# Optimization experiments

Measured on AMD Instinct MI355X. Metric: run time of the kernel, lower is better.

## Reference

```python
import jax, jax.numpy as jnp
import numpy as np
import math

B, S, D = 4, 4096, 512

def setup_inputs() -> dict:
    key = jax.random.key(0)
    k_tok, k1, k2, k3 = jax.random.split(key, 4)
    scale = 1.0 / math.sqrt(D)
    return {
        "token": jax.random.normal(k_tok, (B, S, D), dtype=jnp.float32),
        "W1": jax.random.normal(k1, (D, D), dtype=jnp.float32) * scale,
        "W2": jax.random.normal(k2, (D, D), dtype=jnp.float32) * scale,
        "W3": jax.random.normal(k3, (D, D), dtype=jnp.float32) * scale,
    }

def reference(token, W1, W2, W3):
    # nn.Linear(dim, dim, bias=False): y = x @ W.T; W stored as [out, in]
    q = jnp.einsum('bsd,ed->bse', token, W1)  # t1(token)
    k = jnp.einsum('bsd,ed->bse', token, W2)  # t2(token)
    v = jnp.einsum('bsd,ed->bse', token, W3)  # t3(token)
    logits = jnp.einsum('bse,bte->bst', q, k) / jnp.sqrt(jnp.float32(token.shape[-1]))
    scores = jax.nn.softmax(logits, axis=-1)  # full [B,S,S] materialized, as in source
    return jnp.einsum('bst,bte->bse', scores, v)
```

## Files before the change

kernel.cpp:

```cpp
#include <hip/hip_runtime.h>
#include <stdint.h>


#define BDIM 4
#define SDIM 4096
#define DDIM 512
#define MROWS (BDIM * SDIM)
#define XB_ELEMS ((size_t)MROWS * DDIM)
#define W_ELEMS ((size_t)DDIM * DDIM)

typedef short short8_t __attribute__((ext_vector_type(8)));
typedef short short4_t __attribute__((ext_vector_type(4)));
typedef float float4_t __attribute__((ext_vector_type(4)));

typedef __attribute__((address_space(1))) void gvoid_t;
typedef __attribute__((address_space(3))) void lvoid_t;

__device__ __forceinline__ short f2bf(float f) {
    union { float f; uint32_t u; } v; v.f = f;
    uint32_t r = v.u + 0x7FFFu + ((v.u >> 16) & 1u);
    return (short)(r >> 16);
}
__device__ __forceinline__ float bf2f(short s) {
    union { uint32_t u; float f; } v; v.u = ((uint32_t)(uint16_t)s) << 16;
    return v.f;
}

__global__ void detect_kernel(const uint32_t* __restrict__ tok, int* __restrict__ flag) {
    __shared__ int red[256];
    const int tid = threadIdx.x;
    int c = 0;
    for (int i = tid; i < 4096; i += 256) {
        uint32_t e = (tok[i] >> 7) & 0xFFu;
        c += (e >= 105u && e <= 135u) ? 1 : 0;
    }
    red[tid] = c;
    __syncthreads();
    for (int s = 128; s > 0; s >>= 1) {
        if (tid < s) red[tid] += red[tid + s];
        __syncthreads();
    }
    if (tid == 0) *flag = (red[0] > 2048) ? 1 : 0;
}

__global__ void zero_rs_kernel(float* __restrict__ RS) {
    RS[blockIdx.x * 256 + threadIdx.x] = 0.f;
}

__global__ void convert_kernel(const void* __restrict__ X, const void* __restrict__ W1,
                               const void* __restrict__ W2, const void* __restrict__ W3,
                               short* __restrict__ dst, const int* __restrict__ flagp)
{
    const int bf16in = *flagp;
    const size_t i4 = ((size_t)blockIdx.x * 256 + threadIdx.x) * 4;
    const void* src; size_t off;
    if (i4 < XB_ELEMS) { src = X; off = i4; }
    else {
        const size_t j = i4 - XB_ELEMS;
        const int g = (int)(j / W_ELEMS);
        src = (g == 0) ? W1 : (g == 1) ? W2 : W3;
        off = j - (size_t)g * W_ELEMS;
    }
    if (bf16in) {
        *(short4_t*)(dst + i4) = *(const short4_t*)((const short*)src + off);
    } else {
        float4 v = *(const float4*)((const float*)src + off);
        short4_t s = { f2bf(v.x), f2bf(v.y), f2bf(v.z), f2bf(v.w) };
        *(short4_t*)(dst + i4) = s;
    }
}

__device__ __forceinline__ void gemm_core(
    const short* __restrict__ A, int lda,
    const short* __restrict__ B, int ldb,
    int m0, int n0, int kIters,
    short* As, short* Bs, float4_t acc[4][4])
{
    const int tid = threadIdx.x;
    const int w = tid >> 6, lane = tid & 63, quad = lane >> 4, l16 = lane & 15;
    const int wm = w >> 1, wn = w & 1;
    const int rsub = lane >> 2;
    const int col8 = 8 * (lane & 3);

    for (int kk = 0; kk < kIters; ++kk) {
        const int k0 = 32 * kk;
        __syncthreads();
#pragma unroll
        for (int c = 0; c < 2; ++c) {
            const int row = 32 * w + 16 * c + rsub;
            const short* g = A + (size_t)(m0 + row) * lda + k0 + col8;
            __builtin_amdgcn_global_load_lds((const gvoid_t*)g,
                (lvoid_t*)(As + (32 * w + 16 * c) * 32), 16, 0, 0);
        }
#pragma unroll
        for (int c = 0; c < 2; ++c) {
            const int row = 32 * w + 16 * c + rsub;
            const short* g = B + (size_t)(n0 + row) * ldb + k0 + col8;
            __builtin_amdgcn_global_load_lds((const gvoid_t*)g,
                (lvoid_t*)(Bs + (32 * w + 16 * c) * 32), 16, 0, 0);
        }
        __syncthreads();

        short8_t af[4], bfr[4];
#pragma unroll
        for (int mt = 0; mt < 4; ++mt)
            af[mt] = *(const short8_t*)&As[(64 * wm + 16 * mt + l16) * 32 + 8 * quad];
#pragma unroll
        for (int nt = 0; nt < 4; ++nt)
            bfr[nt] = *(const short8_t*)&Bs[(64 * wn + 16 * nt + l16) * 32 + 8 * quad];
#pragma unroll
        for (int mt = 0; mt < 4; ++mt)
#pragma unroll
            for (int nt = 0; nt < 4; ++nt)
                acc[mt][nt] = __builtin_amdgcn_mfma_f32_16x16x32_bf16(af[mt], bfr[nt], acc[mt][nt], 0, 0, 0);
    }
}

__global__ void proj_fast(const short* __restrict__ XbWb, short* __restrict__ QKV)
{
    __shared__ __align__(16) short As[128 * 32];
    __shared__ __align__(16) short Bs[128 * 32];

    const short* Xb = XbWb;
    const int bid = blockIdx.x;
    const int g = bid >> 9;
    const int r = bid & 511;

    const short* Ap; const short* Bp; short* Op;
    int m0, n0, ldo;
    if (g == 2) {
        Ap = XbWb + XB_ELEMS + 2 * W_ELEMS; Bp = Xb;
        Op = QKV + 2 * (size_t)MROWS * DDIM;
        m0 = 128 * (r & 3); n0 = 128 * (r >> 2); ldo = MROWS;
    } else {
        Ap = Xb; Bp = XbWb + XB_ELEMS + (size_t)g * W_ELEMS;
        Op = QKV + (size_t)g * MROWS * DDIM;
        m0 = 128 * (r >> 2); n0 = 128 * (r & 3); ldo = DDIM;
    }

    const float4_t z4 = {0.f, 0.f, 0.f, 0.f};
    float4_t acc[4][4];
#pragma unroll
    for (int i = 0; i < 4; ++i)
#pragma unroll
        for (int j = 0; j < 4; ++j) acc[i][j] = z4;

    gemm_core(Ap, DDIM, Bp, DDIM, m0, n0, 16, As, Bs, acc);

    const int tid = threadIdx.x;
    const int w = tid >> 6, lane = tid & 63, quad = lane >> 4, l16 = lane & 15;
    const int wm = w >> 1, wn = w & 1;
#pragma unroll
    for (int mt = 0; mt < 4; ++mt)
#pragma unroll
        for (int nt = 0; nt < 4; ++nt)
#pragma unroll
            for (int rr = 0; rr < 4; ++rr) {
                const int m = m0 + 64 * wm + 16 * mt + 4 * quad + rr;
                const int n = n0 + 64 * wn + 16 * nt + l16;
                Op[(size_t)m * ldo + n] = f2bf(acc[mt][nt][rr]);
            }
}

__global__ void qkt_kernel(const short* __restrict__ QKV, short* __restrict__ P,
                           float* __restrict__ RS, int bbase)
{
    __shared__ __align__(16) short As[128 * 32];
    __shared__ __align__(16) short Bs[128 * 32];

    const int bid = blockIdx.x;
    const int bb = bid >> 10;
    const int r = bid & 1023;
    const int b = bbase + bb;
    const int m0 = 128 * (r >> 5);
    const int n0 = 128 * (r & 31);

    const short* Qb = QKV + (size_t)b * SDIM * DDIM;
    const short* Kb = QKV + (size_t)MROWS * DDIM + (size_t)b * SDIM * DDIM;

    const float4_t z4 = {0.f, 0.f, 0.f, 0.f};
    float4_t acc[4][4];
#pragma unroll
    for (int i = 0; i < 4; ++i)
#pragma unroll
        for (int j = 0; j < 4; ++j) acc[i][j] = z4;

    gemm_core(Qb, DDIM, Kb, DDIM, m0, n0, 16, As, Bs, acc);

    const int tid = threadIdx.x;
    const int w = tid >> 6, lane = tid & 63, quad = lane >> 4, l16 = lane & 15;
    const int wm = w >> 1, wn = w & 1;
    const float kSc = 1.44269504088896341f * 0.04419417382415922f;
    short* Pb = P + (size_t)bb * SDIM * SDIM;
#pragma unroll
    for (int mt = 0; mt < 4; ++mt)
#pragma unroll
        for (int rr = 0; rr < 4; ++rr) {
            const int q = m0 + 64 * wm + 16 * mt + 4 * quad + rr;
            float sum = 0.f;
#pragma unroll
            for (int nt = 0; nt < 4; ++nt) {
                const float p = exp2f(acc[mt][nt][rr] * kSc);
                const short pb = f2bf(p);
                sum += bf2f(pb);
                Pb[(size_t)q * SDIM + n0 + 64 * wn + 16 * nt + l16] = pb;
            }
            sum += __shfl_xor(sum, 1); sum += __shfl_xor(sum, 2);
            sum += __shfl_xor(sum, 4); sum += __shfl_xor(sum, 8);
            if (l16 == 0) atomicAdd(&RS[(size_t)b * SDIM + q], sum);
        }
}

__global__ void pv_kernel(const short* __restrict__ P, const short* __restrict__ QKV,
                          const float* __restrict__ RS, void* __restrict__ out,
                          const int* __restrict__ flagp, int bbase)
{
    __shared__ __align__(16) short As[128 * 32];
    __shared__ __align__(16) short Bs[128 * 32];

    const int bf16out = *flagp;
    const int bid = blockIdx.x;
    const int bb = bid >> 7;
    const int r = bid & 127;
    const int b = bbase + bb;
    const int m0 = 128 * (r >> 2);
    const int n0 = 128 * (r & 3);

    const short* Pb = P + (size_t)bb * SDIM * SDIM;
    const short* Vt = QKV + 2 * (size_t)MROWS * DDIM + (size_t)b * SDIM;

    const float4_t z4 = {0.f, 0.f, 0.f, 0.f};
    float4_t acc[4][4];
#pragma unroll
    for (int i = 0; i < 4; ++i)
#pragma unroll
        for (int j = 0; j < 4; ++j) acc[i][j] = z4;

    gemm_core(Pb, SDIM, Vt, MROWS, m0, n0, 128, As, Bs, acc);

    const int tid = threadIdx.x;
    const int w = tid >> 6, lane = tid & 63, quad = lane >> 4, l16 = lane & 15;
    const int wm = w >> 1, wn = w & 1;
#pragma unroll
    for (int mt = 0; mt < 4; ++mt)
#pragma unroll
        for (int rr = 0; rr < 4; ++rr) {
            const size_t grow = (size_t)b * SDIM + m0 + 64 * wm + 16 * mt + 4 * quad + rr;
            const float inv = 1.0f / RS[grow];
#pragma unroll
            for (int nt = 0; nt < 4; ++nt) {
                const int n = n0 + 64 * wn + 16 * nt + l16;
                const float o = acc[mt][nt][rr] * inv;
                if (bf16out) ((short*)out)[grow * DDIM + n] = f2bf(o);
                else         ((float*)out)[grow * DDIM + n] = o;
            }
        }
}

__global__ void proj_mfma_legacy(const void* __restrict__ X, const void* __restrict__ W1,
                          const void* __restrict__ W2, const void* __restrict__ W3,
                          short* __restrict__ QKV, const int* __restrict__ flagp)
{
    __shared__ __align__(16) short As[128][40];
    __shared__ __align__(16) short Bs[128][40];

    const int bf16in = *flagp;
    const int bid = blockIdx.x;
    const int g = bid >> 9;
    const int r = bid & 511;

    const void* Ap; const void* Bp; short* Op;
    int m0, n0, ldo;
    if (g == 2) {
        Ap = W3; Bp = X; Op = QKV + 2 * (size_t)MROWS * DDIM;
        m0 = 128 * (r & 3); n0 = 128 * (r >> 2); ldo = MROWS;
    } else {
        Ap = X; Bp = (g == 0) ? W1 : W2; Op = QKV + (size_t)g * MROWS * DDIM;
        m0 = 128 * (r >> 2); n0 = 128 * (r & 3); ldo = DDIM;
    }

    const float* Af = (const float*)Ap;  const float* Bf = (const float*)Bp;
    const short* Ah = (const short*)Ap;  const short* Bh = (const short*)Bp;

    const int tid = threadIdx.x;
    const int w = tid >> 6, lane = tid & 63, quad = lane >> 4, l16 = lane & 15;
    const int wm = w >> 1, wn = w & 1;
    const int rgrp = tid >> 3, cg = tid & 7;

    const float4_t z4 = {0.f, 0.f, 0.f, 0.f};
    float4_t acc[4][4];
#pragma unroll
    for (int i = 0; i < 4; ++i)
#pragma unroll
        for (int j = 0; j < 4; ++j) acc[i][j] = z4;

    for (int kk = 0; kk < 16; ++kk) {
        const int k0 = 32 * kk;
        __syncthreads();
        if (bf16in) {
#pragma unroll
            for (int i = 0; i < 4; ++i) {
                const int row = rgrp + 32 * i;
                *(short4_t*)&As[row][4 * cg] =
                    *(const short4_t*)(Ah + (size_t)(m0 + row) * DDIM + k0 + 4 * cg);
                *(short4_t*)&Bs[row][4 * cg] =
                    *(const short4_t*)(Bh + (size_t)(n0 + row) * DDIM + k0 + 4 * cg);
            }
        } else {
#pragma unroll
            for (int i = 0; i < 4; ++i) {
                const int row = rgrp + 32 * i;
                float4 va = *(const float4*)(Af + (size_t)(m0 + row) * DDIM + k0 + 4 * cg);
                short4_t sa = { f2bf(va.x), f2bf(va.y), f2bf(va.z), f2bf(va.w) };
                *(short4_t*)&As[row][4 * cg] = sa;
                float4 vb = *(const float4*)(Bf + (size_t)(n0 + row) * DDIM + k0 + 4 * cg);
                short4_t sb = { f2bf(vb.x), f2bf(vb.y), f2bf(vb.z), f2bf(vb.w) };
                *(short4_t*)&Bs[row][4 * cg] = sb;
            }
        }
        __syncthreads();

        short8_t af[4], bfr[4];
#pragma unroll
        for (int mt = 0; mt < 4; ++mt)
            af[mt] = *(const short8_t*)&As[64 * wm + 16 * mt + l16][8 * quad];
#pragma unroll
        for (int nt = 0; nt < 4; ++nt)
            bfr[nt] = *(const short8_t*)&Bs[64 * wn + 16 * nt + l16][8 * quad];
#pragma unroll
        for (int mt = 0; mt < 4; ++mt)
#pragma unroll
            for (int nt = 0; nt < 4; ++nt)
                acc[mt][nt] = __builtin_amdgcn_mfma_f32_16x16x32_bf16(af[mt], bfr[nt], acc[mt][nt], 0, 0, 0);
    }

#pragma unroll
    for (int mt = 0; mt < 4; ++mt)
#pragma unroll
        for (int nt = 0; nt < 4; ++nt)
#pragma unroll
            for (int rr = 0; rr < 4; ++rr) {
                const int m = m0 + 64 * wm + 16 * mt + 4 * quad + rr;
                const int n = n0 + 64 * wn + 16 * nt + l16;
                Op[(size_t)m * ldo + n] = f2bf(acc[mt][nt][rr]);
            }
}

__global__ void attn_mfma(const short* __restrict__ QKV, void* __restrict__ out,
                          const int* __restrict__ flagp)
{
    __shared__ __align__(16) short Ks[32][520];
    __shared__ __align__(16) short Ps[32][72];
    __shared__ float rowsum[2][32];

    const int bf16out = *flagp;
    const short* Qb = QKV;
    const short* Kb = QKV + (size_t)MROWS * DDIM;
    const short* Vt = QKV + 2 * (size_t)MROWS * DDIM;

    const int b = blockIdx.x >> 7;
    const int q0 = (blockIdx.x & 127) * 32;
    const int tid = threadIdx.x;
    const int w = tid >> 6, lane = tid & 63, quad = lane >> 4, l16 = lane & 15;
    const int strip = w >> 1, half = w & 1;

    short8_t qf[16];
    {
        const short* qrow = Qb + (size_t)(b * SDIM + q0 + 16 * strip + l16) * DDIM + 8 * quad;
#pragma unroll
        for (int kc = 0; kc < 16; ++kc)
            qf[kc] = *(const short8_t*)(qrow + 32 * kc);
    }

    const float4_t z4 = {0.f, 0.f, 0.f, 0.f};
    float4_t o[2][8];
#pragma unroll
    for (int mt = 0; mt < 2; ++mt)
#pragma unroll
        for (int nt = 0; nt < 8; ++nt) o[mt][nt] = z4;
    float rs[4] = {0.f, 0.f, 0.f, 0.f};

    const float kSc = 1.44269504088896341f * 0.04419417382415922f;

    for (int kt = 0; kt < 128; ++kt) {
        const int kv0 = 32 * kt;
        __syncthreads();
#pragma unroll
        for (int r = 0; r < 8; ++r) {
            const int kv = 8 * w + r;
            short8_t t = *(const short8_t*)(Kb + (size_t)(b * SDIM + kv0 + kv) * DDIM + 8 * lane);
            *(short8_t*)&Ks[kv][8 * lane] = t;
        }
        __syncthreads();

        float4_t sacc = z4;
#pragma unroll
        for (int kc = 0; kc < 16; ++kc) {
            short8_t kf = *(const short8_t*)&Ks[16 * half + l16][32 * kc + 8 * quad];
            sacc = __builtin_amdgcn_mfma_f32_16x16x32_bf16(qf[kc], kf, sacc, 0, 0, 0);
        }

#pragma unroll
        for (int r = 0; r < 4; ++r) {
            const float p = exp2f(sacc[r] * kSc);
            const short pb = f2bf(p);
            rs[r] += bf2f(pb);
            Ps[16 * strip + 4 * quad + r][16 * half + l16] = pb;
        }
        __syncthreads();

        short8_t pa0 = *(const short8_t*)&Ps[l16][8 * quad];
        short8_t pa1 = *(const short8_t*)&Ps[16 + l16][8 * quad];
#pragma unroll
        for (int nt = 0; nt < 8; ++nt) {
            const short* vp = Vt + (size_t)(128 * w + 16 * nt + l16) * MROWS
                            + (b * SDIM + kv0 + 8 * quad);
            short8_t vb = *(const short8_t*)vp;
            o[0][nt] = __builtin_amdgcn_mfma_f32_16x16x32_bf16(pa0, vb, o[0][nt], 0, 0, 0);
            o[1][nt] = __builtin_amdgcn_mfma_f32_16x16x32_bf16(pa1, vb, o[1][nt], 0, 0, 0);
        }
    }

#pragma unroll
    for (int r = 0; r < 4; ++r) {
        float v = rs[r];
        v += __shfl_xor(v, 1); v += __shfl_xor(v, 2);
        v += __shfl_xor(v, 4); v += __shfl_xor(v, 8);
        rs[r] = v;
    }
    if (l16 == 0) {
#pragma unroll
        for (int r = 0; r < 4; ++r)
            rowsum[half][16 * strip + 4 * quad + r] = rs[r];
    }
    __syncthreads();

#pragma unroll
    for (int mt = 0; mt < 2; ++mt)
#pragma unroll
        for (int r = 0; r < 4; ++r) {
            const int q = 16 * mt + 4 * quad + r;
            const float inv = 1.0f / (rowsum[0][q] + rowsum[1][q]);
            const size_t base = (size_t)(b * SDIM + q0 + q) * DDIM + 128 * w + l16;
            if (bf16out) {
                short* orow = (short*)out + base;
#pragma unroll
                for (int nt = 0; nt < 8; ++nt)
                    orow[16 * nt] = f2bf(o[mt][nt][r] * inv);
            } else {
                float* orow = (float*)out + base;
#pragma unroll
                for (int nt = 0; nt < 8; ++nt)
                    orow[16 * nt] = o[mt][nt][r] * inv;
            }
        }
}

__global__ void zero_out_kernel(short* __restrict__ out, int n) {
    int i = blockIdx.x * 256 + threadIdx.x;
    if (i < n) out[i] = 0;
}

extern "C" void kernel_launch(void* const* d_in, const int* in_sizes, int n_in,
                              void* d_out, int out_size, void* d_ws, size_t ws_size,
                              hipStream_t stream) {
    const void* token = d_in[0];
    const void* Wp[3] = { d_in[1], d_in[2], d_in[3] };
    {
        int wi = 0;
        const void* tk = nullptr; const void* ws3[3] = {nullptr, nullptr, nullptr};
        bool ok = true;
        for (int i = 0; i < n_in && i < 4; ++i) {
            if (in_sizes[i] == BDIM * SDIM * DDIM) { if (tk) ok = false; tk = d_in[i]; }
            else if (in_sizes[i] == DDIM * DDIM) { if (wi < 3) ws3[wi++] = d_in[i]; else ok = false; }
            else ok = false;
        }
        if (ok && tk && wi == 3) { token = tk; Wp[0] = ws3[0]; Wp[1] = ws3[1]; Wp[2] = ws3[2]; }
    }

    const size_t qkvBytes = 3 * (size_t)MROWS * DDIM * sizeof(short);
    const size_t need_base = qkvBytes + 256;
    if (ws_size < need_base) {
        zero_out_kernel<<<(out_size + 255) / 256, 256, 0, stream>>>((short*)d_out, out_size);
        return;
    }

    short* QKV = (short*)d_ws;
    int* flag = (int*)((char*)d_ws + qkvBytes);
    short* P = (short*)((char*)d_ws + need_base);
    const size_t pElems1 = (size_t)SDIM * SDIM;

    int nb = 0;
    for (int cand = 4; cand >= 1; cand >>= 1) {
        const size_t need = need_base + (size_t)cand * pElems1 * sizeof(short)
                          + (size_t)MROWS * sizeof(float);
        if (ws_size >= need) { nb = cand; break; }
    }

    detect_kernel<<<1, 256, 0, stream>>>((const uint32_t*)token, flag);

    if (nb == 0) {
        proj_mfma_legacy<<<dim3(1536), 256, 0, stream>>>(token, Wp[0], Wp[1], Wp[2], QKV, flag);
        attn_mfma<<<dim3(512), 256, 0, stream>>>(QKV, d_out, flag);
        return;
    }

    short* XbWb = P;
    const size_t cvt4 = (XB_ELEMS + 3 * W_ELEMS) / 4;
    convert_kernel<<<dim3((unsigned)(cvt4 / 256)), 256, 0, stream>>>(
        token, Wp[0], Wp[1], Wp[2], XbWb, flag);
    proj_fast<<<dim3(1536), 256, 0, stream>>>(XbWb, QKV);

    float* RS = (float*)(P + (size_t)nb * pElems1);
    zero_rs_kernel<<<dim3(MROWS / 256), 256, 0, stream>>>(RS);
    for (int p = 0; p < BDIM / nb; ++p) {
        const int bbase = p * nb;
        qkt_kernel<<<dim3(nb * 1024), 256, 0, stream>>>(QKV, P, RS, bbase);
        pv_kernel<<<dim3(nb * 128), 256, 0, stream>>>(P, QKV, RS, d_out, flag, bbase);
    }
}
```

Before: 354.6 us.

## Replace QK^T kernel with 256x256 tiled, 8-wave pipelined LDS-direct MFMA kernel

Replaces the 128x128 QK^T tile kernel with a 256x256 tile kernel that uses 512 threads and 128KB of dynamic LDS. The K dimension is split into 64-wide stages, double-buffered through global_load_lds with swizzled layouts and interleaved barriers. The block index is remapped so consecutive blocks spread across XCDs. The larger tile raises reuse of each loaded tile per FLOP and overlaps loads with MFMA, at the cost of fewer, heavier blocks and more register pressure for the 8x4 accumulators.

```diff
diff --git a/kernel.cpp b/kernel.cpp
--- a/kernel.cpp
+++ b/kernel.cpp
@@ -8,6 +8,7 @@
 #define MROWS (BDIM * SDIM)
 #define XB_ELEMS ((size_t)MROWS * DDIM)
 #define W_ELEMS ((size_t)DDIM * DDIM)
+#define KT8 8
 
 typedef short short8_t __attribute__((ext_vector_type(8)));
 typedef short short4_t __attribute__((ext_vector_type(4)));
@@ -162,41 +163,101 @@
             }
 }
 
-__global__ void qkt_kernel(const short* __restrict__ QKV, short* __restrict__ P,
-                           float* __restrict__ RS, int bbase)
-{
-    __shared__ __align__(16) short As[128 * 32];
-    __shared__ __align__(16) short Bs[128 * 32];
-
-    const int bid = blockIdx.x;
-    const int bb = bid >> 10;
-    const int r = bid & 1023;
+__global__ void qkt8_kernel(const short* __restrict__ QKV, short* __restrict__ P,
+                            float* __restrict__ RS, int bbase)
+{
+    extern __shared__ short lds[];
+
+    const int cpx = (int)(gridDim.x >> 3);
+    const int bid = (int)blockIdx.x;
+    const int l = (bid & 7) * cpx + (bid >> 3);
+    const int bb = l >> 8;
+    const int r = l & 255;
     const int b = bbase + bb;
-    const int m0 = 128 * (r >> 5);
-    const int n0 = 128 * (r & 31);
+    const int m0 = 256 * (r >> 4);
+    const int n0 = 256 * (r & 15);
 
     const short* Qb = QKV + (size_t)b * SDIM * DDIM;
     const short* Kb = QKV + (size_t)MROWS * DDIM + (size_t)b * SDIM * DDIM;
 
+    const int tid = (int)threadIdx.x;
+    const int w = tid >> 6, lane = tid & 63;
+    const int quad = lane >> 4, l16 = lane & 15;
+    const int wm = w >> 2, wn = w & 3;
+    const int xsw = (l16 >> 1) & 3;
+    const int sg = (lane & 3) ^ ((lane >> 3) & 3);
+
+    auto STAGE = [&](int u, int ab, int kh) {
+        if (u >= KT8) return;
+        const short* gb = ab ? Kb : Qb;
+        const int r0 = ab ? n0 : m0;
+        short* rg = lds + (size_t)((u & 1) * 4 + ab * 2 + kh) * 8192;
+#pragma unroll
+        for (int j = 0; j < 2; ++j) {
+            const int row = j * 128 + 16 * w + (lane >> 2);
+            const short* g = gb + (size_t)(r0 + row) * DDIM + u * 64 + kh * 32 + 8 * sg;
+            __builtin_amdgcn_global_load_lds((const gvoid_t*)g,
+                (lvoid_t*)(rg + (j * 128 + 16 * w) * 32), 16, 0, 0);
+        }
+    };
+
     const float4_t z4 = {0.f, 0.f, 0.f, 0.f};
-    float4_t acc[4][4];
-#pragma unroll
-    for (int i = 0; i < 4; ++i)
+    float4_t acc[8][4];
+#pragma unroll
+    for (int i = 0; i < 8; ++i)
 #pragma unroll
         for (int j = 0; j < 4; ++j) acc[i][j] = z4;
 
-    gemm_core(Qb, DDIM, Kb, DDIM, m0, n0, 16, As, Bs, acc);
-
-    const int tid = threadIdx.x;
-    const int w = tid >> 6, lane = tid & 63, quad = lane >> 4, l16 = lane & 15;
-    const int wm = w >> 1, wn = w & 1;
+    STAGE(0, 0, 0); STAGE(0, 1, 0); STAGE(0, 0, 1); STAGE(0, 1, 1);
+    STAGE(1, 0, 0); STAGE(1, 1, 0);
+    asm volatile("s_waitcnt vmcnt(4)" ::: "memory");
+    __builtin_amdgcn_s_barrier();
+
+    short8_t af[8];
+    for (int t = 0; t < KT8; ++t) {
+        const int d = t & 1;
+#pragma unroll
+        for (int ks = 0; ks < 2; ++ks) {
+            const short* Ar = lds + (size_t)(d * 4 + ks) * 8192;
+            const short* Br = lds + (size_t)(d * 4 + 2 + ks) * 8192;
+#pragma unroll
+            for (int nh = 0; nh < 2; ++nh) {
+                if (nh == 0) {
+#pragma unroll
+                    for (int mt = 0; mt < 8; ++mt)
+                        af[mt] = *(const short8_t*)&Ar[(128 * wm + 16 * mt + l16) * 32 + 8 * (quad ^ xsw)];
+                }
+                const short8_t bf0 = *(const short8_t*)&Br[(64 * wn + 32 * nh + l16) * 32 + 8 * (quad ^ xsw)];
+                const short8_t bf1 = *(const short8_t*)&Br[(64 * wn + 32 * nh + 16 + l16) * 32 + 8 * (quad ^ xsw)];
+                const int ph = ks * 2 + nh;
+                if (ph == 0)      STAGE(t + 1, 0, 1);
+                else if (ph == 1) STAGE(t + 1, 1, 1);
+                else if (ph == 2) STAGE(t + 2, 0, 0);
+                else              STAGE(t + 2, 1, 0);
+                __builtin_amdgcn_s_barrier();
+                __builtin_amdgcn_s_setprio(1);
+#pragma unroll
+                for (int mt = 0; mt < 8; ++mt) {
+                    acc[mt][2 * nh + 0] = __builtin_amdgcn_mfma_f32_16x16x32_bf16(af[mt], bf0, acc[mt][2 * nh + 0], 0, 0, 0);
+                    acc[mt][2 * nh + 1] = __builtin_amdgcn_mfma_f32_16x16x32_bf16(af[mt], bf1, acc[mt][2 * nh + 1], 0, 0, 0);
+                }
+                __builtin_amdgcn_s_setprio(0);
+                if (ph == 3) {
+                    if (t < KT8 - 2) asm volatile("s_waitcnt vmcnt(4)" ::: "memory");
+                    else             asm volatile("s_waitcnt vmcnt(0)" ::: "memory");
+                }
+                __builtin_amdgcn_s_barrier();
+            }
+        }
+    }
+
     const float kSc = 1.44269504088896341f * 0.04419417382415922f;
     short* Pb = P + (size_t)bb * SDIM * SDIM;
 #pragma unroll
-    for (int mt = 0; mt < 4; ++mt)
+    for (int mt = 0; mt < 8; ++mt)
 #pragma unroll
         for (int rr = 0; rr < 4; ++rr) {
-            const int q = m0 + 64 * wm + 16 * mt + 4 * quad + rr;
+            const int q = m0 + 128 * wm + 16 * mt + 4 * quad + rr;
             float sum = 0.f;
 #pragma unroll
             for (int nt = 0; nt < 4; ++nt) {
@@ -505,6 +566,13 @@
         return;
     }
 
+    static bool qkt8_attr = false;
+    if (!qkt8_attr) {
+        (void)hipFuncSetAttribute(reinterpret_cast<const void*>(qkt8_kernel),
+                                  hipFuncAttributeMaxDynamicSharedMemorySize, 131072);
+        qkt8_attr = true;
+    }
+
     short* XbWb = P;
     const size_t cvt4 = (XB_ELEMS + 3 * W_ELEMS) / 4;
     convert_kernel<<<dim3((unsigned)(cvt4 / 256)), 256, 0, stream>>>(
@@ -515,7 +583,7 @@
     zero_rs_kernel<<<dim3(MROWS / 256), 256, 0, stream>>>(RS);
     for (int p = 0; p < BDIM / nb; ++p) {
         const int bbase = p * nb;
-        qkt_kernel<<<dim3(nb * 1024), 256, 0, stream>>>(QKV, P, RS, bbase);
+        qkt8_kernel<<<dim3(nb * 256), 512, 131072, stream>>>(QKV, P, RS, bbase);
         pv_kernel<<<dim3(nb * 128), 256, 0, stream>>>(P, QKV, RS, d_out, flag, bbase);
     }
 }
```

New measurement: 992.4 us. 2.8x slower.

## Widen QK^T and PV tiles to 256x128 with 512-thread blocks and XCD swizzle

Applied to the files above, without the earlier changes.

Adds a gemm_core_wide routine in which each 512-thread block (8 waves) computes a 256x128 output tile. This halves the number of B-tile loads per output and the number of blocks in both the QK^T and PV kernels. Block indices are remapped round-robin across 8 groups so that neighbouring tiles land on the same XCD and share L2 better. In exchange the block is larger and uses more LDS, which may reduce occupancy, and the epilogue indexing must still match the new wave layout.

```diff
diff --git a/kernel.cpp b/kernel.cpp
--- a/kernel.cpp
+++ b/kernel.cpp
@@ -98,6 +98,51 @@
             const short* g = B + (size_t)(n0 + row) * ldb + k0 + col8;
             __builtin_amdgcn_global_load_lds((const gvoid_t*)g,
                 (lvoid_t*)(Bs + (32 * w + 16 * c) * 32), 16, 0, 0);
+        }
+        __syncthreads();
+
+        short8_t af[4], bfr[4];
+#pragma unroll
+        for (int mt = 0; mt < 4; ++mt)
+            af[mt] = *(const short8_t*)&As[(64 * wm + 16 * mt + l16) * 32 + 8 * quad];
+#pragma unroll
+        for (int nt = 0; nt < 4; ++nt)
+            bfr[nt] = *(const short8_t*)&Bs[(64 * wn + 16 * nt + l16) * 32 + 8 * quad];
+#pragma unroll
+        for (int mt = 0; mt < 4; ++mt)
+#pragma unroll
+            for (int nt = 0; nt < 4; ++nt)
+                acc[mt][nt] = __builtin_amdgcn_mfma_f32_16x16x32_bf16(af[mt], bfr[nt], acc[mt][nt], 0, 0, 0);
+    }
+}
+
+__device__ __forceinline__ void gemm_core_wide(
+    const short* __restrict__ A, int lda,
+    const short* __restrict__ B, int ldb,
+    int m0, int n0, int kIters,
+    short* As , short* Bs , float4_t acc[4][4])
+{
+    const int tid = threadIdx.x;
+    const int w = tid >> 6, lane = tid & 63, quad = lane >> 4, l16 = lane & 15;
+    const int wm = w >> 1, wn = w & 1;
+    const int rsub = lane >> 2;
+    const int col8 = 8 * (lane & 3);
+
+    for (int kk = 0; kk < kIters; ++kk) {
+        const int k0 = 32 * kk;
+        __syncthreads();
+#pragma unroll
+        for (int c = 0; c < 2; ++c) {
+            const int row = 128 * c + 16 * w + rsub;
+            const short* g = A + (size_t)(m0 + row) * lda + k0 + col8;
+            __builtin_amdgcn_global_load_lds((const gvoid_t*)g,
+                (lvoid_t*)(As + (128 * c + 16 * w) * 32), 16, 0, 0);
+        }
+        {
+            const int row = 16 * w + rsub;
+            const short* g = B + (size_t)(n0 + row) * ldb + k0 + col8;
+            __builtin_amdgcn_global_load_lds((const gvoid_t*)g,
+                (lvoid_t*)(Bs + (16 * w) * 32), 16, 0, 0);
         }
         __syncthreads();
 
@@ -165,14 +210,16 @@
 __global__ void qkt_kernel(const short* __restrict__ QKV, short* __restrict__ P,
                            float* __restrict__ RS, int bbase)
 {
-    __shared__ __align__(16) short As[128 * 32];
+    __shared__ __align__(16) short As[256 * 32];
     __shared__ __align__(16) short Bs[128 * 32];
 
-    const int bid = blockIdx.x;
-    const int bb = bid >> 10;
-    const int r = bid & 1023;
+    const int cpx = (int)(gridDim.x >> 3);
+    const int bid = (int)blockIdx.x;
+    const int l = (bid & 7) * cpx + (bid >> 3);
+    const int bb = l >> 9;
+    const int r = l & 511;
     const int b = bbase + bb;
-    const int m0 = 128 * (r >> 5);
+    const int m0 = 256 * (r >> 5);
     const int n0 = 128 * (r & 31);
 
     const short* Qb = QKV + (size_t)b * SDIM * DDIM;
@@ -185,7 +232,7 @@
 #pragma unroll
         for (int j = 0; j < 4; ++j) acc[i][j] = z4;
 
-    gemm_core(Qb, DDIM, Kb, DDIM, m0, n0, 16, As, Bs, acc);
+    gemm_core_wide(Qb, DDIM, Kb, DDIM, m0, n0, 16, As, Bs, acc);
 
     const int tid = threadIdx.x;
     const int w = tid >> 6, lane = tid & 63, quad = lane >> 4, l16 = lane & 15;
@@ -215,15 +262,17 @@
                           const float* __restrict__ RS, void* __restrict__ out,
                           const int* __restrict__ flagp, int bbase)
 {
-    __shared__ __align__(16) short As[128 * 32];
+    __shared__ __align__(16) short As[256 * 32];
     __shared__ __align__(16) short Bs[128 * 32];
 
     const int bf16out = *flagp;
-    const int bid = blockIdx.x;
-    const int bb = bid >> 7;
-    const int r = bid & 127;
+    const int cpx = (int)(gridDim.x >> 3);
+    const int bid = (int)blockIdx.x;
+    const int l = (bid & 7) * cpx + (bid >> 3);
+    const int bb = l >> 6;
+    const int r = l & 63;
     const int b = bbase + bb;
-    const int m0 = 128 * (r >> 2);
+    const int m0 = 256 * (r >> 2);
     const int n0 = 128 * (r & 3);
 
     const short* Pb = P + (size_t)bb * SDIM * SDIM;
@@ -236,7 +285,7 @@
 #pragma unroll
         for (int j = 0; j < 4; ++j) acc[i][j] = z4;
 
-    gemm_core(Pb, SDIM, Vt, MROWS, m0, n0, 128, As, Bs, acc);
+    gemm_core_wide(Pb, SDIM, Vt, MROWS, m0, n0, 128, As, Bs, acc);
 
     const int tid = threadIdx.x;
     const int w = tid >> 6, lane = tid & 63, quad = lane >> 4, l16 = lane & 15;
@@ -515,7 +564,7 @@
     zero_rs_kernel<<<dim3(MROWS / 256), 256, 0, stream>>>(RS);
     for (int p = 0; p < BDIM / nb; ++p) {
         const int bbase = p * nb;
-        qkt_kernel<<<dim3(nb * 1024), 256, 0, stream>>>(QKV, P, RS, bbase);
-        pv_kernel<<<dim3(nb * 128), 256, 0, stream>>>(P, QKV, RS, d_out, flag, bbase);
-    }
-}
+        qkt_kernel<<<dim3(nb * 512), 512, 0, stream>>>(QKV, P, RS, bbase);
+        pv_kernel<<<dim3(nb * 64), 512, 0, stream>>>(P, QKV, RS, d_out, flag, bbase);
+    }
+}
```

Result: slower. 386.0 us (+8.9%).

## Double-buffer LDS tiles in shared GEMM core to overlap loads with MFMA

Applied to the files above, without the earlier changes.

The shared GEMM core now keeps two LDS buffers for the A and B tiles. It issues the async global-to-LDS load for the next K-slice before running the MFMAs on the current one, so each K step needs one barrier instead of two. This targets the memory-latency stalls in the projection, QK^T and PV kernels. In exchange, shared memory per block doubles, which may lower occupancy.

```diff
diff --git a/kernel.cpp b/kernel.cpp
--- a/kernel.cpp
+++ b/kernel.cpp
@@ -82,44 +82,54 @@
     const int rsub = lane >> 2;
     const int col8 = 8 * (lane & 3);
 
-    for (int kk = 0; kk < kIters; ++kk) {
+    auto STAGE = [&](int d, int kk) {
         const int k0 = 32 * kk;
-        __syncthreads();
+        short* Asd = As + d * 4096;
+        short* Bsd = Bs + d * 4096;
 #pragma unroll
         for (int c = 0; c < 2; ++c) {
             const int row = 32 * w + 16 * c + rsub;
             const short* g = A + (size_t)(m0 + row) * lda + k0 + col8;
             __builtin_amdgcn_global_load_lds((const gvoid_t*)g,
-                (lvoid_t*)(As + (32 * w + 16 * c) * 32), 16, 0, 0);
+                (lvoid_t*)(Asd + (32 * w + 16 * c) * 32), 16, 0, 0);
         }
 #pragma unroll
         for (int c = 0; c < 2; ++c) {
             const int row = 32 * w + 16 * c + rsub;
             const short* g = B + (size_t)(n0 + row) * ldb + k0 + col8;
             __builtin_amdgcn_global_load_lds((const gvoid_t*)g,
-                (lvoid_t*)(Bs + (32 * w + 16 * c) * 32), 16, 0, 0);
-        }
-        __syncthreads();
-
+                (lvoid_t*)(Bsd + (32 * w + 16 * c) * 32), 16, 0, 0);
+        }
+    };
+
+    STAGE(0, 0);
+    __syncthreads();
+    int cur = 0;
+    for (int kk = 0; kk < kIters; ++kk) {
+        if (kk + 1 < kIters) STAGE(cur ^ 1, kk + 1);
+        const short* Asd = As + cur * 4096;
+        const short* Bsd = Bs + cur * 4096;
         short8_t af[4], bfr[4];
 #pragma unroll
         for (int mt = 0; mt < 4; ++mt)
-            af[mt] = *(const short8_t*)&As[(64 * wm + 16 * mt + l16) * 32 + 8 * quad];
+            af[mt] = *(const short8_t*)&Asd[(64 * wm + 16 * mt + l16) * 32 + 8 * quad];
 #pragma unroll
         for (int nt = 0; nt < 4; ++nt)
-            bfr[nt] = *(const short8_t*)&Bs[(64 * wn + 16 * nt + l16) * 32 + 8 * quad];
+            bfr[nt] = *(const short8_t*)&Bsd[(64 * wn + 16 * nt + l16) * 32 + 8 * quad];
 #pragma unroll
         for (int mt = 0; mt < 4; ++mt)
 #pragma unroll
             for (int nt = 0; nt < 4; ++nt)
                 acc[mt][nt] = __builtin_amdgcn_mfma_f32_16x16x32_bf16(af[mt], bfr[nt], acc[mt][nt], 0, 0, 0);
+        __syncthreads();
+        cur ^= 1;
     }
 }
 
 __global__ void proj_fast(const short* __restrict__ XbWb, short* __restrict__ QKV)
 {
-    __shared__ __align__(16) short As[128 * 32];
-    __shared__ __align__(16) short Bs[128 * 32];
+    __shared__ __align__(16) short As[2 * 128 * 32];
+    __shared__ __align__(16) short Bs[2 * 128 * 32];
 
     const short* Xb = XbWb;
     const int bid = blockIdx.x;
@@ -165,8 +175,8 @@
 __global__ void qkt_kernel(const short* __restrict__ QKV, short* __restrict__ P,
                            float* __restrict__ RS, int bbase)
 {
-    __shared__ __align__(16) short As[128 * 32];
-    __shared__ __align__(16) short Bs[128 * 32];
+    __shared__ __align__(16) short As[2 * 128 * 32];
+    __shared__ __align__(16) short Bs[2 * 128 * 32];
 
     const int bid = blockIdx.x;
     const int bb = bid >> 10;
@@ -215,8 +225,8 @@
                           const float* __restrict__ RS, void* __restrict__ out,
                           const int* __restrict__ flagp, int bbase)
 {
-    __shared__ __align__(16) short As[128 * 32];
-    __shared__ __align__(16) short Bs[128 * 32];
+    __shared__ __align__(16) short As[2 * 128 * 32];
+    __shared__ __align__(16) short Bs[2 * 128 * 32];
 
     const int bf16out = *flagp;
     const int bid = blockIdx.x;
```

Result: slower. 373.9 us (+5.4%).
